# Performance work log

Measured on AMD Instinct MI355X. Metric: run time of the kernel, lower is better.

Reference implementation:

```python
import jax, jax.numpy as jnp
import numpy as np

T, B, S, D = 512, 32, 512, 512
EPS = 1e-6  # LayerNorm eps


def _ln(x, g, b):
    m = jnp.mean(x, axis=-1, keepdims=True)
    v = jnp.mean((x - m) ** 2, axis=-1, keepdims=True)
    return g * (x - m) * jax.lax.rsqrt(v + EPS) + b


def setup_inputs() -> dict:
    key = jax.random.key(0)
    ks = jax.random.split(key, 10)
    sc = 1.0 / np.sqrt(D).astype(np.float32)
    return {
        "prev_layer": jax.random.normal(ks[0], (T, B, D), jnp.float32),
        "hidden": jax.random.normal(ks[1], (B, D), jnp.float32),
        "enc_output": jax.random.normal(ks[2], (B, S, D), jnp.float32),
        "memory_length": jax.random.randint(ks[3], (B,), 1, S + 1),
        # nn.Linear weights stored as [in, out] (transposed torch layout)
        "W_in": jax.random.normal(ks[4], (D, 3 * D), jnp.float32) * sc,
        "W_enc": jax.random.normal(ks[5], (D, D), jnp.float32) * sc,
        "W_attn_in": jax.random.normal(ks[6], (D, D), jnp.float32) * sc,
        "W_hidden": jax.random.normal(ks[7], (D, D), jnp.float32) * sc,
        "W_ctx": jax.random.normal(ks[8], (D, D), jnp.float32) * sc,
        # LayerNorm gains/biases (5 LNs)
        "g_pre": jnp.ones((3 * D,), jnp.float32), "b_pre": jnp.zeros((3 * D,), jnp.float32),
        "g_enc": jnp.ones((D,), jnp.float32), "b_enc": jnp.zeros((D,), jnp.float32),
        "g_attn": jnp.ones((D,), jnp.float32), "b_attn": jnp.zeros((D,), jnp.float32),
        "g_h": jnp.ones((D,), jnp.float32), "b_h": jnp.zeros((D,), jnp.float32),
        "g_c": jnp.ones((D,), jnp.float32), "b_c": jnp.zeros((D,), jnp.float32),
    }


def reference(prev_layer, hidden, enc_output, W_in, W_enc, W_attn_in, W_hidden,
              W_ctx, g_pre, b_pre, g_enc, b_enc, g_attn, b_attn, g_h, b_h,
              g_c, b_c, memory_length):
    d = prev_layer.shape[-1]
    sqrt_d = jnp.sqrt(jnp.asarray(d, prev_layer.dtype))
    # dropout is identity in eval mode
    preact = _ln(prev_layer @ W_in, g_pre, b_pre)          # [T,B,3D]
    pctx = _ln(enc_output @ W_enc, g_enc, b_enc)           # [B,S,D]
    z, h_gate, pl_t = jnp.split(preact, 3, axis=-1)
    z = jax.nn.sigmoid(z)
    h_gate = jax.nn.sigmoid(h_gate)

    # SRU-style linear recurrence: s_t = (1-z_t)*s_{t-1} + z_t*pl_t
    def step(h, zp):
        z_t, p_t = zp
        s = (1.0 - z_t) * h + z_t * p_t
        return s, s

    hidden_last, ss = jax.lax.scan(step, hidden, (z, pl_t))  # ss: [T,B,D]

    attn_in = _ln(ss @ W_attn_in, g_attn, b_attn)            # [T,B,D]
    align = jnp.einsum('tbd,bsd->bts', attn_in, pctx)        # [B,T,S]
    mask = jnp.arange(pctx.shape[1])[None, :] < memory_length[:, None]  # [B,S]
    align = jnp.where(mask[:, None, :], align, -jnp.inf)
    av = jax.nn.softmax(align / sqrt_d, axis=-1)             # [B,T,S]
    c = jnp.einsum('bts,bsd->tbd', av, pctx)                 # [T,B,D]
    attn_out = c / sqrt_d

    trans = _ln(ss @ W_hidden, g_h, b_h) + _ln(attn_out @ W_ctx, g_c, b_c)
    out = jnp.tanh(trans)
    out = (1.0 - h_gate) * out + h_gate * prev_layer         # [T,B,D]
    p_attn = jnp.transpose(av, (1, 0, 2))                    # [T,B,S]
    return out, hidden_last, p_attn
```

## Files before the change

### kernel.cpp

```cpp
#include <hip/hip_runtime.h>
#include <hip/hip_bf16.h>
#include <cmath>

#define T_ 512
#define B_ 32
#define S_ 512
#define D_ 512
#define D3_ 1536
#define NCH 16
#define CT (T_ / NCH)
static constexpr float LN_EPS = 1e-6f;
static constexpr float RSQRT_D = 0.044194173824159216f;

typedef __attribute__((ext_vector_type(8))) __bf16 bf16x8;
typedef __attribute__((ext_vector_type(4))) float f32x4;

struct __align__(8) bfx4 { __hip_bfloat16 x, y, z, w; };
struct __align__(16) u16x8 { unsigned short h[8]; };

__device__ __forceinline__ void g2l16(const void* g, void* l) {
    __builtin_amdgcn_global_load_lds(
        (const __attribute__((address_space(1))) unsigned int*)g,
        (__attribute__((address_space(3))) unsigned int*)l, 16, 0, 0);
}

__device__ __forceinline__ float xr_sum16(float v) {
    v += __shfl_xor(v, 1); v += __shfl_xor(v, 2);
    v += __shfl_xor(v, 4); v += __shfl_xor(v, 8); return v;
}
__device__ __forceinline__ float xr_max16(float v) {
    v = fmaxf(v, __shfl_xor(v, 1)); v = fmaxf(v, __shfl_xor(v, 2));
    v = fmaxf(v, __shfl_xor(v, 4)); v = fmaxf(v, __shfl_xor(v, 8)); return v;
}

__device__ __forceinline__ float sigmoidf_(float x) {
    return 1.f / (1.f + __expf(-x));
}
__device__ __forceinline__ float sigmoid_fast(float x) {
    return __fdividef(1.f, 1.f + __expf(-x));
}
__device__ __forceinline__ float tanh_fast(float x) {
    return 1.f - __fdividef(2.f, __expf(2.f * x) + 1.f);
}
__device__ __forceinline__ float bfu(unsigned short u) {
    unsigned int v = ((unsigned int)u) << 16;
    return __uint_as_float(v);
}

__global__ __launch_bounds__(256) void gemm_pre(
    const __hip_bfloat16* __restrict__ A,
    const __hip_bfloat16* __restrict__ Bw,
    __hip_bfloat16* __restrict__ preb,
    float2* __restrict__ part)
{
    __shared__ char smem[32768];

    const int lin = blockIdx.y * 12 + blockIdx.x;
    const int swz = (lin & 7) * 192 + (lin >> 3);
    const int bx = swz % 12, by = swz / 12;
    const int m0 = by * 128, n0 = bx * 128;
    const int tid = threadIdx.x, lane = tid & 63, w = tid >> 6;
    const int wm = (w >> 1) * 64, wn = (w & 1) * 64;
    const int srow = lane >> 2, skB = (lane & 3) * 16;
    const int q = lane >> 4, c = lane & 15;

    f32x4 acc[4][4];
#pragma unroll
    for (int i = 0; i < 4; i++)
#pragma unroll
        for (int j = 0; j < 4; j++) acc[i][j] = (f32x4)(0.0f);

    const char* ga0 = (const char*)(A + (long)(m0 + w * 16 + srow) * 512) + skB;
    const char* ga1 = (const char*)(A + (long)(m0 + (w + 4) * 16 + srow) * 512) + skB;
    const char* gb0 = (const char*)(Bw + (long)(n0 + w * 16 + srow) * 512) + skB;
    const char* gb1 = (const char*)(Bw + (long)(n0 + (w + 4) * 16 + srow) * 512) + skB;
    char* la0 = smem + w * 1024 + lane * 16;
    char* la1 = smem + (w + 4) * 1024 + lane * 16;
    char* lb0 = smem + 8192 + w * 1024 + lane * 16;
    char* lb1 = smem + 8192 + (w + 4) * 1024 + lane * 16;
    const char* Ar = smem + (wm + c) * 64 + q * 16;
    const char* Br = smem + 8192 + (wn + c) * 64 + q * 16;

    g2l16(ga0, la0);
    g2l16(ga1, la1);
    g2l16(gb0, lb0);
    g2l16(gb1, lb1);
    __syncthreads();

#pragma unroll
    for (int kk = 0; kk < 16; kk++) {
        const int cb = (kk & 1) << 14;
        const int nb = cb ^ 16384;
        if (kk < 15) {
            const long kb = (long)(kk + 1) * 64;
            g2l16(ga0 + kb, la0 + nb);
            g2l16(ga1 + kb, la1 + nb);
            g2l16(gb0 + kb, lb0 + nb);
            g2l16(gb1 + kb, lb1 + nb);
        }
        bf16x8 af[4], bfr[4];
#pragma unroll
        for (int i = 0; i < 4; i++) {
            af[i] = *(const bf16x8*)(Ar + cb + i * 1024);
            bfr[i] = *(const bf16x8*)(Br + cb + i * 1024);
        }
#pragma unroll
        for (int i = 0; i < 4; i++)
#pragma unroll
            for (int j = 0; j < 4; j++)
                acc[i][j] = __builtin_amdgcn_mfma_f32_16x16x32_bf16(
                    af[i], bfr[j], acc[i][j], 0, 0, 0);
        __syncthreads();
    }

    float2* sred = (float2*)smem;
#pragma unroll
    for (int i = 0; i < 4; i++)
#pragma unroll
        for (int r = 0; r < 4; r++) {
            float s = 0.f, qq = 0.f;
#pragma unroll
            for (int j = 0; j < 4; j++) {
                float v = acc[i][j][r]; s += v; qq += v * v;
            }
            s = xr_sum16(s); qq = xr_sum16(qq);
            if (c == 0) sred[(wm + i * 16 + q * 4 + r) * 2 + (w & 1)] =
                make_float2(s, qq);
        }
    __syncthreads();
    if ((w & 1) == 0 && c == 0) {
#pragma unroll
        for (int i = 0; i < 4; i++)
#pragma unroll
            for (int r = 0; r < 4; r++) {
                int row = wm + i * 16 + q * 4 + r;
                float2 a = sred[row * 2], b2 = sred[row * 2 + 1];
                part[(long)bx * 16384 + m0 + row] =
                    make_float2(a.x + b2.x, a.y + b2.y);
            }
    }
    __syncthreads();

    for (int p = 0; p < 2; p++) {
        if ((w >> 1) == p) {
#pragma unroll
            for (int i = 0; i < 4; i++)
#pragma unroll
                for (int j = 0; j < 4; j++)
#pragma unroll
                    for (int r = 0; r < 4; r++) {
                        int row = i * 16 + q * 4 + r;
                        int col = wn + j * 16 + c;
                        ((__hip_bfloat16*)smem)[row * 128 + col] =
                            __float2bfloat16(acc[i][j][r]);
                    }
        }
        __syncthreads();
#pragma unroll
        for (int rnd = 0; rnd < 4; rnd++) {
            int row = rnd * 16 + (tid >> 4);
            int ch = tid & 15;
            uint4 v = *(const uint4*)(smem + row * 256 + ch * 16);
            long grow = m0 + p * 64 + row;
            *(uint4*)((char*)preb + grow * 3072 + (long)n0 * 2 + ch * 16) = v;
        }
        __syncthreads();
    }
}

__global__ __launch_bounds__(256) void g128(
    const __hip_bfloat16* __restrict__ A, long ldaE,
    const __hip_bfloat16* __restrict__ Bw, long bStrideZ,
    __hip_bfloat16* __restrict__ out, long outStrideB,
    float2* __restrict__ part, float scale, int swizzle)
{
    __shared__ char smem[32768];
    int bx, by;
    if (gridDim.z > 1) {
        bx = blockIdx.x; by = blockIdx.y;
        A += (long)blockIdx.z * 512;
        Bw += (long)blockIdx.z * bStrideZ;
        out += (long)blockIdx.z * 512;
    } else if (swizzle) {
        const int nwg = gridDim.x * gridDim.y;
        const int lin = blockIdx.y * gridDim.x + blockIdx.x;
        const int cpx = nwg >> 3;
        const int swz = (lin & 7) * cpx + (lin >> 3);
        bx = swz % gridDim.x; by = swz / gridDim.x;
    } else { bx = blockIdx.x; by = blockIdx.y; }

    const int m0 = by * 128, n0 = bx * 128;
    const int tid = threadIdx.x, lane = tid & 63, w = tid >> 6;
    const int wm = (w >> 1) * 64, wn = (w & 1) * 64;
    const int srow = lane >> 2, skB = (lane & 3) * 16;
    const int q = lane >> 4, c = lane & 15;

    f32x4 acc[4][4];
#pragma unroll
    for (int i = 0; i < 4; i++)
#pragma unroll
        for (int j = 0; j < 4; j++) acc[i][j] = (f32x4)(0.0f);

    const char* ga0 = (const char*)(A + (long)(m0 + w * 16 + srow) * ldaE) + skB;
    const char* ga1 = (const char*)(A + (long)(m0 + (w + 4) * 16 + srow) * ldaE) + skB;
    const char* gb0 = (const char*)(Bw + (long)(n0 + w * 16 + srow) * 512) + skB;
    const char* gb1 = (const char*)(Bw + (long)(n0 + (w + 4) * 16 + srow) * 512) + skB;
    char* la0 = smem + w * 1024 + lane * 16;
    char* la1 = smem + (w + 4) * 1024 + lane * 16;
    char* lb0 = smem + 8192 + w * 1024 + lane * 16;
    char* lb1 = smem + 8192 + (w + 4) * 1024 + lane * 16;
    const char* Ar = smem + (wm + c) * 64 + q * 16;
    const char* Br = smem + 8192 + (wn + c) * 64 + q * 16;

    g2l16(ga0, la0);
    g2l16(ga1, la1);
    g2l16(gb0, lb0);
    g2l16(gb1, lb1);
    __syncthreads();

#pragma unroll
    for (int kk = 0; kk < 16; kk++) {
        const int cb = (kk & 1) << 14;
        const int nb = cb ^ 16384;
        if (kk < 15) {
            const long kb = (long)(kk + 1) * 64;
            g2l16(ga0 + kb, la0 + nb);
            g2l16(ga1 + kb, la1 + nb);
            g2l16(gb0 + kb, lb0 + nb);
            g2l16(gb1 + kb, lb1 + nb);
        }
        bf16x8 af[4], bfr[4];
#pragma unroll
        for (int i = 0; i < 4; i++) {
            af[i] = *(const bf16x8*)(Ar + cb + i * 1024);
            bfr[i] = *(const bf16x8*)(Br + cb + i * 1024);
        }
#pragma unroll
        for (int i = 0; i < 4; i++)
#pragma unroll
            for (int j = 0; j < 4; j++)
                acc[i][j] = __builtin_amdgcn_mfma_f32_16x16x32_bf16(
                    af[i], bfr[j], acc[i][j], 0, 0, 0);
        __syncthreads();
    }

    if (part) {
        float2* sred = (float2*)smem;
#pragma unroll
        for (int i = 0; i < 4; i++)
#pragma unroll
            for (int r = 0; r < 4; r++) {
                float s = 0.f, qq = 0.f;
#pragma unroll
                for (int j = 0; j < 4; j++) {
                    float v = acc[i][j][r]; s += v; qq += v * v;
                }
                s = xr_sum16(s); qq = xr_sum16(qq);
                if (c == 0) sred[(wm + i * 16 + q * 4 + r) * 2 + (w & 1)] =
                    make_float2(s, qq);
            }
        __syncthreads();
        if ((w & 1) == 0 && c == 0) {
#pragma unroll
            for (int i = 0; i < 4; i++)
#pragma unroll
                for (int r = 0; r < 4; r++) {
                    int row = wm + i * 16 + q * 4 + r;
                    float2 a = sred[row * 2], b2 = sred[row * 2 + 1];
                    part[(long)bx * 16384 + m0 + row] =
                        make_float2(a.x + b2.x, a.y + b2.y);
                }
        }
        __syncthreads();
    }

    for (int p = 0; p < 2; p++) {
        if ((w >> 1) == p) {
#pragma unroll
            for (int i = 0; i < 4; i++)
#pragma unroll
                for (int j = 0; j < 4; j++)
#pragma unroll
                    for (int r = 0; r < 4; r++) {
                        int row = i * 16 + q * 4 + r;
                        int col = wn + j * 16 + c;
                        ((__hip_bfloat16*)smem)[row * 128 + col] =
                            __float2bfloat16(acc[i][j][r] * scale);
                    }
        }
        __syncthreads();
#pragma unroll
        for (int rnd = 0; rnd < 4; rnd++) {
            int row = rnd * 16 + (tid >> 4);
            int ch = tid & 15;
            uint4 v = *(const uint4*)(smem + row * 256 + ch * 16);
            long grow = m0 + p * 64 + row;
            *(uint4*)((char*)out + grow * outStrideB + (long)n0 * 2 + ch * 16) = v;
        }
        __syncthreads();
    }
}

#define RC_BUF 34816
__device__ __forceinline__ void rows_core32_lds(
    const __hip_bfloat16* A, long lda,
    const __hip_bfloat16* B, long ldb,
    char* smem, f32x4 (&acc)[2][8])
{
    const int tid = threadIdx.x, lane = tid & 63, w = tid >> 6;
#pragma unroll
    for (int m = 0; m < 2; m++)
#pragma unroll
        for (int j = 0; j < 8; j++) acc[m][j] = (f32x4)(0.0f);

    const char* ga = (const char*)(A + (long)(w * 16 + (lane >> 2)) * lda) + (lane & 3) * 16;
    char* la = smem + w * 1024 + lane * 16;
    const char* gb = (const char*)(B + (long)(w * 128 + (lane >> 2)) * ldb) + (lane & 3) * 16;
    char* lb = smem + 2048 + w * 8192 + lane * 16;
    const long ldbB16 = (long)ldb * 32;
    const char* Ar = smem + (lane & 15) * 64 + (lane >> 4) * 16;
    const char* Br = smem + 2048 + (w * 128 + (lane & 15)) * 64 + (lane >> 4) * 16;

    if (w < 2) g2l16(ga, la);
#pragma unroll
    for (int s = 0; s < 8; s++) g2l16(gb + s * ldbB16, lb + s * 1024);
    __syncthreads();

#pragma unroll
    for (int kk = 0; kk < 16; kk++) {
        const int cb = (kk & 1) * RC_BUF;
        const int nb = ((kk & 1) ^ 1) * RC_BUF;
        if (kk < 15) {
            const long kb = (long)(kk + 1) * 64;
            if (w < 2) g2l16(ga + kb, la + nb);
#pragma unroll
            for (int s = 0; s < 8; s++)
                g2l16(gb + kb + s * ldbB16, lb + nb + s * 1024);
        }
        bf16x8 af[2], bfr[8];
#pragma unroll
        for (int m = 0; m < 2; m++) af[m] = *(const bf16x8*)(Ar + cb + m * 1024);
#pragma unroll
        for (int j = 0; j < 8; j++) bfr[j] = *(const bf16x8*)(Br + cb + j * 1024);
#pragma unroll
        for (int m = 0; m < 2; m++)
#pragma unroll
            for (int j = 0; j < 8; j++)
                acc[m][j] = __builtin_amdgcn_mfma_f32_16x16x32_bf16(
                    af[m], bfr[j], acc[m][j], 0, 0, 0);
        __syncthreads();
    }
}

__global__ __launch_bounds__(256, 2) void gemm_attn(
    const __hip_bfloat16* __restrict__ attninC2,
    const __hip_bfloat16* __restrict__ pctxb,
    const int* __restrict__ mlen,
    float* __restrict__ pattn, __hip_bfloat16* __restrict__ softb)
{
    __shared__ char smem[69632];
    const int b = blockIdx.z;
    const long t0 = (long)blockIdx.y * 32;
    f32x4 acc[2][8];
    rows_core32_lds(attninC2 + (long)b * 1024 + t0 * 32768, 32768,
                    pctxb + (long)b * 262144, 512, smem, acc);

    const int tid = threadIdx.x, lane = tid & 63, w = tid >> 6;
    const int q = lane >> 4, c = lane & 15;
    const int len = mlen[b];
    float* sred = (float*)smem;

#pragma unroll
    for (int m = 0; m < 2; m++)
#pragma unroll
        for (int r = 0; r < 4; r++) {
            float mx = -INFINITY;
#pragma unroll
            for (int j = 0; j < 8; j++) {
                int col = w * 128 + j * 16 + c;
                float v = acc[m][j][r] * RSQRT_D;
                acc[m][j][r] = v;
                if (col < len) mx = fmaxf(mx, v);
            }
            mx = xr_max16(mx);
            if (c == 0) sred[(m * 16 + q * 4 + r) * 4 + w] = mx;
        }
    __syncthreads();
    float rmax[2][4];
#pragma unroll
    for (int m = 0; m < 2; m++)
#pragma unroll
        for (int r = 0; r < 4; r++) {
            int row = m * 16 + q * 4 + r;
            rmax[m][r] = fmaxf(fmaxf(sred[row * 4], sred[row * 4 + 1]),
                               fmaxf(sred[row * 4 + 2], sred[row * 4 + 3]));
        }
    __syncthreads();
#pragma unroll
    for (int m = 0; m < 2; m++)
#pragma unroll
        for (int r = 0; r < 4; r++) {
            float s = 0.f;
#pragma unroll
            for (int j = 0; j < 8; j++) {
                int col = w * 128 + j * 16 + c;
                float e = (col < len) ? __expf(acc[m][j][r] - rmax[m][r]) : 0.f;
                acc[m][j][r] = e; s += e;
            }
            s = xr_sum16(s);
            if (c == 0) sred[(m * 16 + q * 4 + r) * 4 + w] = s;
        }
    __syncthreads();
    float rinv[2][4];
#pragma unroll
    for (int m = 0; m < 2; m++)
#pragma unroll
        for (int r = 0; r < 4; r++) {
            int row = m * 16 + q * 4 + r;
            rinv[m][r] = 1.f / (sred[row * 4] + sred[row * 4 + 1] +
                                sred[row * 4 + 2] + sred[row * 4 + 3]);
        }
    __syncthreads();

#pragma unroll
    for (int m = 0; m < 2; m++)
#pragma unroll
        for (int j = 0; j < 8; j++)
#pragma unroll
            for (int r = 0; r < 4; r++) {
                int row = m * 16 + q * 4 + r;
                int col = w * 128 + j * 16 + c;
                float p = acc[m][j][r] * rinv[m][r];
                acc[m][j][r] = p;
                pattn[((t0 + row) * 32 + b) * 512 + col] = p;
                ((__hip_bfloat16*)smem)[row * 512 + col] = __float2bfloat16(p);
            }
    __syncthreads();
#pragma unroll
    for (int rnd = 0; rnd < 8; rnd++) {
        int row = rnd * 4 + w;
        uint4 v = *(const uint4*)(smem + row * 1024 + lane * 16);
        *(uint4*)((char*)softb + ((t0 + row) * 32 + b) * 1024 + lane * 16) = v;
    }
}

__global__ __launch_bounds__(256) void stats4(
    const float2* __restrict__ part, float2* __restrict__ st)
{
    int r = blockIdx.x * 256 + threadIdx.x;
    float s = 0.f, qq = 0.f;
#pragma unroll
    for (int cb = 0; cb < 4; cb++) {
        float2 v = part[(long)cb * 16384 + r]; s += v.x; qq += v.y;
    }
    float m = s * (1.f / 512);
    float rs = rsqrtf(qq * (1.f / 512) - m * m + LN_EPS);
    st[r] = make_float2(m, rs);
}

__global__ __launch_bounds__(256) void ln_apply_s(
    __hip_bfloat16* __restrict__ x,
    const float2* __restrict__ st,
    const float* __restrict__ g, const float* __restrict__ bb)
{
    int i = blockIdx.x * 256 + threadIdx.x;
    int row = i >> 6;
    int c0 = (i & 63) * 8;
    float2 s = st[row];
    char* p = (char*)x + (long)row * 2048 + (long)(i & 63) * 16;
    u16x8 v = *(const u16x8*)p;
    float4 g0 = *(const float4*)(g + c0), g1 = *(const float4*)(g + c0 + 4);
    float4 b0 = *(const float4*)(bb + c0), b1 = *(const float4*)(bb + c0 + 4);
    float gv[8] = {g0.x, g0.y, g0.z, g0.w, g1.x, g1.y, g1.z, g1.w};
    float bv[8] = {b0.x, b0.y, b0.z, b0.w, b1.x, b1.y, b1.z, b1.w};
#pragma unroll
    for (int k = 0; k < 8; k++) {
        float f = (bfu(v.h[k]) - s.x) * s.y * gv[k] + bv[k];
        v.h[k] = __hip_bfloat16_raw(__float2bfloat16(f)).x;
    }
    *(u16x8*)p = v;
}

__global__ __launch_bounds__(256) void lnt(
    __hip_bfloat16* __restrict__ x,
    __hip_bfloat16* __restrict__ xT,
    const float2* __restrict__ st,
    const float* __restrict__ g, const float* __restrict__ bb)
{
    long boff = (long)blockIdx.z * (S_ * D_);
    int d0 = blockIdx.x * 32, s0 = blockIdx.y * 32;
    __shared__ __hip_bfloat16 t[32][34];
    int tx = threadIdx.x & 31, ty = threadIdx.x >> 5;
    float gv = g[d0 + tx], bv = bb[d0 + tx];
#pragma unroll
    for (int i = 0; i < 4; i++) {
        int srow = s0 + ty + i * 8;
        long row = (long)blockIdx.z * S_ + srow;
        float2 s = st[row];
        float f = (bfu(__hip_bfloat16_raw(x[boff + (long)srow * D_ + d0 + tx]).x)
                   - s.x) * s.y * gv + bv;
        __hip_bfloat16 h = __float2bfloat16(f);
        t[ty + i * 8][tx] = h;
        x[boff + (long)srow * D_ + d0 + tx] = h;
    }
    __syncthreads();
#pragma unroll
    for (int i = 0; i < 4; i++)
        xT[boff + (long)(d0 + ty + i * 8) * S_ + s0 + tx] = t[tx][ty + i * 8];
}

__global__ __launch_bounds__(256) void fin_ep(
    const __hip_bfloat16* __restrict__ h2r,
    const __hip_bfloat16* __restrict__ C2,
    const __hip_bfloat16* __restrict__ preb,
    const float2* __restrict__ st_c, const float2* __restrict__ st_h,
    const float2* __restrict__ st_p,
    const float* __restrict__ g_c, const float* __restrict__ b_c,
    const float* __restrict__ g_h, const float* __restrict__ b_h,
    const float* __restrict__ g_pre, const float* __restrict__ b_pre,
    const float* __restrict__ prev, float* __restrict__ out)
{
    const long m0 = (long)blockIdx.x * 32;
    const int tid = threadIdx.x;
#pragma unroll
    for (int ch = 0; ch < 16; ch++) {
        int f4 = ch * 256 + tid;
        int row = f4 >> 7;
        long rowg = m0 + row;
        int col = (f4 & 127) * 4;
        ushort4 h2 = *(const ushort4*)((const char*)h2r + rowg * 1024 + col * 2);
        ushort4 h1 = *(const ushort4*)((const char*)C2 + rowg * 2048 + 1024 + col * 2);
        ushort4 hr = *(const ushort4*)((const char*)preb + rowg * 3072 + 1024 + col * 2);
        float4 pv = *(const float4*)(prev + rowg * 512 + col);
        float4 gc = *(const float4*)(g_c + col), bc = *(const float4*)(b_c + col);
        float4 gh = *(const float4*)(g_h + col), bh = *(const float4*)(b_h + col);
        float4 gp = *(const float4*)(g_pre + 512 + col);
        float4 bp = *(const float4*)(b_pre + 512 + col);
        float2 sc = st_c[rowg], sh = st_h[rowg], sp = st_p[rowg];
        auto fuse = [&](unsigned short h2u, unsigned short h1u, unsigned short hru,
                        float pvv, float gcv, float bcv, float ghv, float bhv,
                        float gpv, float bpv) -> float {
            float t2 = (bfu(h2u) - sc.x) * sc.y * gcv + bcv;
            float t1 = (bfu(h1u) - sh.x) * sh.y * ghv + bhv;
            float hg = sigmoid_fast((bfu(hru) - sp.x) * sp.y * gpv + bpv);
            return (1.f - hg) * tanh_fast(t1 + t2) + hg * pvv;
        };
        float4 o;
        o.x = fuse(h2.x, h1.x, hr.x, pv.x, gc.x, bc.x, gh.x, bh.x, gp.x, bp.x);
        o.y = fuse(h2.y, h1.y, hr.y, pv.y, gc.y, bc.y, gh.y, bh.y, gp.y, bp.y);
        o.z = fuse(h2.z, h1.z, hr.z, pv.z, gc.z, bc.z, gh.z, bh.z, gp.z, bp.z);
        o.w = fuse(h2.w, h1.w, hr.w, pv.w, gc.w, bc.w, gh.w, bh.w, gp.w, bp.w);
        *(float4*)(out + rowg * 512 + col) = o;
    }
}

__global__ __launch_bounds__(256) void cvt4(
    const float* __restrict__ x, __hip_bfloat16* __restrict__ y, int n4)
{
    int i = blockIdx.x * 256 + threadIdx.x;
    if (i >= n4) return;
    float4 v = ((const float4*)x)[i];
    bfx4 o;
    o.x = __float2bfloat16(v.x); o.y = __float2bfloat16(v.y);
    o.z = __float2bfloat16(v.z); o.w = __float2bfloat16(v.w);
    ((bfx4*)y)[i] = o;
}

__global__ __launch_bounds__(256) void wtrans(
    const float* __restrict__ w0, const float* __restrict__ w1,
    const float* __restrict__ w2, const float* __restrict__ w3,
    const float* __restrict__ w4, __hip_bfloat16* __restrict__ WT)
{
    int z = blockIdx.z;
    const float* W; long off; int N;
    if (z == 0)      { W = w0; off = 0;                N = 1536; }
    else if (z == 1) { W = w1; off = 786432;           N = 512; }
    else if (z == 2) { W = w2; off = 786432 + 262144;  N = 512; }
    else if (z == 3) { W = w3; off = 786432 + 524288;  N = 512; }
    else             { W = w4; off = 786432 + 786432;  N = 512; }
    int n0 = blockIdx.x * 32, k0 = blockIdx.y * 32;
    if (n0 >= N) return;
    __shared__ float t[32][33];
    int tx = threadIdx.x & 31, ty = threadIdx.x >> 5;
#pragma unroll
    for (int i = 0; i < 4; i++)
        t[ty + i * 8][tx] = W[(long)(k0 + ty + i * 8) * N + n0 + tx];
    __syncthreads();
    __hip_bfloat16* O = WT + off;
#pragma unroll
    for (int i = 0; i < 4; i++)
        O[(long)(n0 + ty + i * 8) * 512 + k0 + tx] =
            __float2bfloat16(t[tx][ty + i * 8]);
}

__global__ __launch_bounds__(256) void stats_fin(
    const float2* __restrict__ part, float2* __restrict__ stats)
{
    int r = blockIdx.x * 256 + threadIdx.x;
    float s = 0.f, qq = 0.f;
#pragma unroll
    for (int cb = 0; cb < 12; cb++) {
        float2 v = part[(long)cb * 16384 + r]; s += v.x; qq += v.y;
    }
    float m = s * (1.f / 1536);
    float rs = rsqrtf(qq * (1.f / 1536) - m * m + LN_EPS);
    stats[r] = make_float2(m, rs);
}

__global__ __launch_bounds__(256) void scan_part1(
    const __hip_bfloat16* __restrict__ preb, const float2* __restrict__ stats,
    const float* __restrict__ gpre, const float* __restrict__ bpre,
    float* __restrict__ Ap, float* __restrict__ Bp)
{
    int i2 = blockIdx.x * 256 + threadIdx.x;
    int b = i2 >> 8, d = (i2 & 255) * 2;
    int idx = b * 512 + d;
    int ch = blockIdx.y;
    float2 gz = *(const float2*)(gpre + d), bz = *(const float2*)(bpre + d);
    float2 gp = *(const float2*)(gpre + 1024 + d);
    float2 bp = *(const float2*)(bpre + 1024 + d);
    float A0 = 1.f, s0 = 0.f, A1 = 1.f, s1 = 0.f;
    for (int t = ch * CT; t < (ch + 1) * CT; t++) {
        long row = (long)t * 32 + b;
        float2 st = stats[row];
        ushort2 zr = *(const ushort2*)(preb + row * 1536 + d);
        ushort2 pr = *(const ushort2*)(preb + row * 1536 + 1024 + d);
        float z0 = sigmoidf_((bfu(zr.x) - st.x) * st.y * gz.x + bz.x);
        float z1 = sigmoidf_((bfu(zr.y) - st.x) * st.y * gz.y + bz.y);
        float p0 = (bfu(pr.x) - st.x) * st.y * gp.x + bp.x;
        float p1 = (bfu(pr.y) - st.x) * st.y * gp.y + bp.y;
        A0 *= (1.f - z0); s0 = (1.f - z0) * s0 + z0 * p0;
        A1 *= (1.f - z1); s1 = (1.f - z1) * s1 + z1 * p1;
    }
    *(float2*)(Ap + ch * 16384 + idx) = make_float2(A0, A1);
    *(float2*)(Bp + ch * 16384 + idx) = make_float2(s0, s1);
}

__global__ __launch_bounds__(256) void scan_part2(
    const float* __restrict__ Ap, const float* __restrict__ Bp,
    const float* __restrict__ h0, float* __restrict__ sin_,
    float* __restrict__ hlast)
{
    int idx = blockIdx.x * 256 + threadIdx.x;
    float s = h0[idx];
    for (int ch = 0; ch < NCH; ch++) {
        sin_[ch * 16384 + idx] = s;
        s = Ap[ch * 16384 + idx] * s + Bp[ch * 16384 + idx];
    }
    hlast[idx] = s;
}

__global__ __launch_bounds__(256) void scan_part3(
    const __hip_bfloat16* __restrict__ preb, const float2* __restrict__ stats,
    const float* __restrict__ gpre, const float* __restrict__ bpre,
    const float* __restrict__ sin_, __hip_bfloat16* __restrict__ ssb)
{
    int i2 = blockIdx.x * 256 + threadIdx.x;
    int b = i2 >> 8, d = (i2 & 255) * 2;
    int idx = b * 512 + d;
    int ch = blockIdx.y;
    float2 gz = *(const float2*)(gpre + d), bz = *(const float2*)(bpre + d);
    float2 gp = *(const float2*)(gpre + 1024 + d);
    float2 bp = *(const float2*)(bpre + 1024 + d);
    float2 sv = *(const float2*)(sin_ + ch * 16384 + idx);
    float s0 = sv.x, s1 = sv.y;
    for (int t = ch * CT; t < (ch + 1) * CT; t++) {
        long row = (long)t * 32 + b;
        float2 st = stats[row];
        ushort2 zr = *(const ushort2*)(preb + row * 1536 + d);
        ushort2 pr = *(const ushort2*)(preb + row * 1536 + 1024 + d);
        float z0 = sigmoidf_((bfu(zr.x) - st.x) * st.y * gz.x + bz.x);
        float z1 = sigmoidf_((bfu(zr.y) - st.x) * st.y * gz.y + bz.y);
        float p0 = (bfu(pr.x) - st.x) * st.y * gp.x + bp.x;
        float p1 = (bfu(pr.y) - st.x) * st.y * gp.y + bp.y;
        s0 += z0 * (p0 - s0);
        s1 += z1 * (p1 - s1);
        ushort2 o;
        o.x = __hip_bfloat16_raw(__float2bfloat16(s0)).x;
        o.y = __hip_bfloat16_raw(__float2bfloat16(s1)).x;
        *(ushort2*)(ssb + (long)t * 16384 + idx) = o;
    }
}

extern "C" void kernel_launch(void* const* d_in, const int* in_sizes, int n_in,
                              void* d_out, int out_size, void* d_ws, size_t ws_size,
                              hipStream_t stream) {
    const float* prev  = (const float*)d_in[0];
    const float* hid0  = (const float*)d_in[1];
    const float* enc   = (const float*)d_in[2];
    const int*   mlen  = (const int*)  d_in[3];
    const float* W_in  = (const float*)d_in[4];
    const float* W_enc = (const float*)d_in[5];
    const float* W_att = (const float*)d_in[6];
    const float* W_hid = (const float*)d_in[7];
    const float* W_ctx = (const float*)d_in[8];
    const float* g_pre = (const float*)d_in[9];
    const float* b_pre = (const float*)d_in[10];
    const float* g_enc = (const float*)d_in[11];
    const float* b_enc = (const float*)d_in[12];
    const float* g_att = (const float*)d_in[13];
    const float* b_att = (const float*)d_in[14];
    const float* g_h   = (const float*)d_in[15];
    const float* b_h   = (const float*)d_in[16];
    const float* g_c   = (const float*)d_in[17];
    const float* b_c   = (const float*)d_in[18];

    float* out   = (float*)d_out;
    float* hlast = out + (long)T_ * B_ * D_;
    float* pattn = hlast + (long)B_ * D_;

    char* ws = (char*)d_ws;
    __hip_bfloat16* preb    = (__hip_bfloat16*)(ws);
    __hip_bfloat16* WT      = (__hip_bfloat16*)(ws + 50331648);
    __hip_bfloat16* prevb   = (__hip_bfloat16*)(ws + 54525952);
    __hip_bfloat16* encb    = (__hip_bfloat16*)(ws + 71303168);
    __hip_bfloat16* pctxb   = (__hip_bfloat16*)(ws + 88080384);
    __hip_bfloat16* pctxT   = (__hip_bfloat16*)(ws + 104857600);
    __hip_bfloat16* ssb     = (__hip_bfloat16*)(ws + 121634816);
    __hip_bfloat16* C2      = (__hip_bfloat16*)(ws + 138412032);
    __hip_bfloat16* attnoutb= (__hip_bfloat16*)(ws + 171966464);
    __hip_bfloat16* softb   = (__hip_bfloat16*)(ws + 188743680);
    float2* part            = (float2*)(ws + 205520896);
    float2* stats           = (float2*)(ws + 207093760);
    float* scanA            = (float*)(ws + 207224832);
    float* scanB            = (float*)(ws + 208273408);
    float* sinb             = (float*)(ws + 209321984);
    float2* stats_enc       = (float2*)(ws + 210370560);
    float2* stats_att       = (float2*)(ws + 210501632);
    float2* stats_h         = (float2*)(ws + 210632704);
    float2* stats_c         = (float2*)(ws + 210763776);

    __hip_bfloat16* h2raw = softb;

    const __hip_bfloat16* W_encT = WT + 786432;
    const __hip_bfloat16* W_attT = WT + 786432 + 262144;
    const __hip_bfloat16* W_ctxT = WT + 786432 + 786432;

    dim3 blk(256);

    cvt4<<<8192, blk, 0, stream>>>(prev, prevb, 2097152);
    cvt4<<<8192, blk, 0, stream>>>(enc, encb, 2097152);
    wtrans<<<dim3(48, 16, 5), blk, 0, stream>>>(W_in, W_enc, W_att, W_hid,
                                                W_ctx, WT);

    gemm_pre<<<dim3(12, 128), blk, 0, stream>>>(prevb, WT, preb, part);
    stats_fin<<<64, blk, 0, stream>>>(part, stats);

    scan_part1<<<dim3(32, NCH), blk, 0, stream>>>(preb, stats, g_pre, b_pre,
                                                  scanA, scanB);
    scan_part2<<<64, blk, 0, stream>>>(scanA, scanB, hid0, sinb, hlast);
    scan_part3<<<dim3(32, NCH), blk, 0, stream>>>(preb, stats, g_pre, b_pre,
                                                  sinb, ssb);

    g128<<<dim3(4, 128), blk, 0, stream>>>(encb, 512, W_encT, 0, pctxb, 1024,
                                           part, 1.f, 1);
    stats4<<<64, blk, 0, stream>>>(part, stats_enc);
    lnt<<<dim3(16, 16, 32), blk, 0, stream>>>(pctxb, pctxT, stats_enc,
                                              g_enc, b_enc);

    g128<<<dim3(8, 128), blk, 0, stream>>>(ssb, 512, W_attT, 0, C2, 2048,
                                           part, 1.f, 1);
    stats4<<<64, blk, 0, stream>>>(part, stats_att);
    stats4<<<64, blk, 0, stream>>>(part + 4 * 16384, stats_h);
    ln_apply_s<<<4096, blk, 0, stream>>>(C2, stats_att, g_att, b_att);

    gemm_attn<<<dim3(1, 16, 32), blk, 0, stream>>>(C2, pctxb, mlen,
                                                   pattn, softb);

    g128<<<dim3(4, 4, 32), blk, 0, stream>>>(softb, 16384, pctxT, 262144,
                                             attnoutb, 32768, nullptr,
                                             RSQRT_D, 0);

    g128<<<dim3(4, 128), blk, 0, stream>>>(attnoutb, 512, W_ctxT, 0, h2raw,
                                           1024, part, 1.f, 1);
    stats4<<<64, blk, 0, stream>>>(part, stats_c);

    fin_ep<<<512, blk, 0, stream>>>(h2raw, C2, preb, stats_c, stats_h, stats,
                                    g_c, b_c, g_h, b_h, g_pre, b_pre, prev,
                                    out);
}
```

Measured before the change: 436.2 us.

## Fold W_ctx into LN-encoded context to drop attention-output GEMM

Uses associativity: (av·pctx)·W_ctx = av·(pctx·W_ctx), and pctx·W_ctx is computed as LN-expanded encoder GEMM with a precomputed (g_enc∘W_ctx)-scaled W_enc product plus rank-one correction vectors u,v. The encoder GEMM now produces both pctx and the projected context in one wide GEMM, fused into a single launch with the ss·[W_att|W_hid] GEMM, and the final W_ctx GEMM on attention output is eliminated. It also unifies gemm_pre into the shared g128 body. This trades one T×B×D×D GEMM for a wider encoder GEMM and adds extra bf16 rounding of the fused weights, a numerical risk.

```diff
diff --git a/kernel.cpp b/kernel.cpp
--- a/kernel.cpp
+++ b/kernel.cpp
@@ -6,7 +6,6 @@
 #define B_ 32
 #define S_ 512
 #define D_ 512
-#define D3_ 1536
 #define NCH 16
 #define CT (T_ / NCH)
 static constexpr float LN_EPS = 1e-6f;
@@ -47,148 +46,14 @@
     return __uint_as_float(v);
 }
 
-__global__ __launch_bounds__(256) void gemm_pre(
-    const __hip_bfloat16* __restrict__ A,
+__device__ __forceinline__ void g128_body(
+    const __hip_bfloat16* __restrict__ A, long ldaE,
     const __hip_bfloat16* __restrict__ Bw,
-    __hip_bfloat16* __restrict__ preb,
-    float2* __restrict__ part)
+    __hip_bfloat16* __restrict__ out, long outStrideB,
+    float2* __restrict__ part, int partMul, int partBase,
+    float scale, int bx, int by)
 {
     __shared__ char smem[32768];
-
-    const int lin = blockIdx.y * 12 + blockIdx.x;
-    const int swz = (lin & 7) * 192 + (lin >> 3);
-    const int bx = swz % 12, by = swz / 12;
-    const int m0 = by * 128, n0 = bx * 128;
-    const int tid = threadIdx.x, lane = tid & 63, w = tid >> 6;
-    const int wm = (w >> 1) * 64, wn = (w & 1) * 64;
-    const int srow = lane >> 2, skB = (lane & 3) * 16;
-    const int q = lane >> 4, c = lane & 15;
-
-    f32x4 acc[4][4];
-#pragma unroll
-    for (int i = 0; i < 4; i++)
-#pragma unroll
-        for (int j = 0; j < 4; j++) acc[i][j] = (f32x4)(0.0f);
-
-    const char* ga0 = (const char*)(A + (long)(m0 + w * 16 + srow) * 512) + skB;
-    const char* ga1 = (const char*)(A + (long)(m0 + (w + 4) * 16 + srow) * 512) + skB;
-    const char* gb0 = (const char*)(Bw + (long)(n0 + w * 16 + srow) * 512) + skB;
-    const char* gb1 = (const char*)(Bw + (long)(n0 + (w + 4) * 16 + srow) * 512) + skB;
-    char* la0 = smem + w * 1024 + lane * 16;
-    char* la1 = smem + (w + 4) * 1024 + lane * 16;
-    char* lb0 = smem + 8192 + w * 1024 + lane * 16;
-    char* lb1 = smem + 8192 + (w + 4) * 1024 + lane * 16;
-    const char* Ar = smem + (wm + c) * 64 + q * 16;
-    const char* Br = smem + 8192 + (wn + c) * 64 + q * 16;
-
-    g2l16(ga0, la0);
-    g2l16(ga1, la1);
-    g2l16(gb0, lb0);
-    g2l16(gb1, lb1);
-    __syncthreads();
-
-#pragma unroll
-    for (int kk = 0; kk < 16; kk++) {
-        const int cb = (kk & 1) << 14;
-        const int nb = cb ^ 16384;
-        if (kk < 15) {
-            const long kb = (long)(kk + 1) * 64;
-            g2l16(ga0 + kb, la0 + nb);
-            g2l16(ga1 + kb, la1 + nb);
-            g2l16(gb0 + kb, lb0 + nb);
-            g2l16(gb1 + kb, lb1 + nb);
-        }
-        bf16x8 af[4], bfr[4];
-#pragma unroll
-        for (int i = 0; i < 4; i++) {
-            af[i] = *(const bf16x8*)(Ar + cb + i * 1024);
-            bfr[i] = *(const bf16x8*)(Br + cb + i * 1024);
-        }
-#pragma unroll
-        for (int i = 0; i < 4; i++)
-#pragma unroll
-            for (int j = 0; j < 4; j++)
-                acc[i][j] = __builtin_amdgcn_mfma_f32_16x16x32_bf16(
-                    af[i], bfr[j], acc[i][j], 0, 0, 0);
-        __syncthreads();
-    }
-
-    float2* sred = (float2*)smem;
-#pragma unroll
-    for (int i = 0; i < 4; i++)
-#pragma unroll
-        for (int r = 0; r < 4; r++) {
-            float s = 0.f, qq = 0.f;
-#pragma unroll
-            for (int j = 0; j < 4; j++) {
-                float v = acc[i][j][r]; s += v; qq += v * v;
-            }
-            s = xr_sum16(s); qq = xr_sum16(qq);
-            if (c == 0) sred[(wm + i * 16 + q * 4 + r) * 2 + (w & 1)] =
-                make_float2(s, qq);
-        }
-    __syncthreads();
-    if ((w & 1) == 0 && c == 0) {
-#pragma unroll
-        for (int i = 0; i < 4; i++)
-#pragma unroll
-            for (int r = 0; r < 4; r++) {
-                int row = wm + i * 16 + q * 4 + r;
-                float2 a = sred[row * 2], b2 = sred[row * 2 + 1];
-                part[(long)bx * 16384 + m0 + row] =
-                    make_float2(a.x + b2.x, a.y + b2.y);
-            }
-    }
-    __syncthreads();
-
-    for (int p = 0; p < 2; p++) {
-        if ((w >> 1) == p) {
-#pragma unroll
-            for (int i = 0; i < 4; i++)
-#pragma unroll
-                for (int j = 0; j < 4; j++)
-#pragma unroll
-                    for (int r = 0; r < 4; r++) {
-                        int row = i * 16 + q * 4 + r;
-                        int col = wn + j * 16 + c;
-                        ((__hip_bfloat16*)smem)[row * 128 + col] =
-                            __float2bfloat16(acc[i][j][r]);
-                    }
-        }
-        __syncthreads();
-#pragma unroll
-        for (int rnd = 0; rnd < 4; rnd++) {
-            int row = rnd * 16 + (tid >> 4);
-            int ch = tid & 15;
-            uint4 v = *(const uint4*)(smem + row * 256 + ch * 16);
-            long grow = m0 + p * 64 + row;
-            *(uint4*)((char*)preb + grow * 3072 + (long)n0 * 2 + ch * 16) = v;
-        }
-        __syncthreads();
-    }
-}
-
-__global__ __launch_bounds__(256) void g128(
-    const __hip_bfloat16* __restrict__ A, long ldaE,
-    const __hip_bfloat16* __restrict__ Bw, long bStrideZ,
-    __hip_bfloat16* __restrict__ out, long outStrideB,
-    float2* __restrict__ part, float scale, int swizzle)
-{
-    __shared__ char smem[32768];
-    int bx, by;
-    if (gridDim.z > 1) {
-        bx = blockIdx.x; by = blockIdx.y;
-        A += (long)blockIdx.z * 512;
-        Bw += (long)blockIdx.z * bStrideZ;
-        out += (long)blockIdx.z * 512;
-    } else if (swizzle) {
-        const int nwg = gridDim.x * gridDim.y;
-        const int lin = blockIdx.y * gridDim.x + blockIdx.x;
-        const int cpx = nwg >> 3;
-        const int swz = (lin & 7) * cpx + (lin >> 3);
-        bx = swz % gridDim.x; by = swz / gridDim.x;
-    } else { bx = blockIdx.x; by = blockIdx.y; }
-
     const int m0 = by * 128, n0 = bx * 128;
     const int tid = threadIdx.x, lane = tid & 63, w = tid >> 6;
     const int wm = (w >> 1) * 64, wn = (w & 1) * 64;
@@ -253,7 +118,7 @@
                 float s = 0.f, qq = 0.f;
 #pragma unroll
                 for (int j = 0; j < 4; j++) {
-                    float v = acc[i][j][r]; s += v; qq += v * v;
+                    float v = acc[i][j][r] * scale; s += v; qq += v * v;
                 }
                 s = xr_sum16(s); qq = xr_sum16(qq);
                 if (c == 0) sred[(wm + i * 16 + q * 4 + r) * 2 + (w & 1)] =
@@ -267,7 +132,7 @@
                 for (int r = 0; r < 4; r++) {
                     int row = wm + i * 16 + q * 4 + r;
                     float2 a = sred[row * 2], b2 = sred[row * 2 + 1];
-                    part[(long)bx * 16384 + m0 + row] =
+                    part[(long)bx * 16384 + (long)(m0 + row) * partMul + partBase] =
                         make_float2(a.x + b2.x, a.y + b2.y);
                 }
         }
@@ -299,6 +164,49 @@
         }
         __syncthreads();
     }
+}
+
+__global__ __launch_bounds__(256) void g128(
+    const __hip_bfloat16* __restrict__ A, long ldaE,
+    const __hip_bfloat16* __restrict__ Bw, long bStrideZ,
+    __hip_bfloat16* __restrict__ out, long outStrideB,
+    float2* __restrict__ part, float scale, int swizzle)
+{
+    int bx, by, pmul = 1, pbase = 0;
+    if (gridDim.z > 1) {
+        bx = blockIdx.x; by = blockIdx.y;
+        A += (long)blockIdx.z * 512;
+        Bw += (long)blockIdx.z * bStrideZ;
+        out += (long)blockIdx.z * 512;
+        pmul = 32; pbase = blockIdx.z;
+    } else if (swizzle) {
+        const int nwg = gridDim.x * gridDim.y;
+        const int lin = blockIdx.y * gridDim.x + blockIdx.x;
+        const int cpx = nwg >> 3;
+        const int swz = (lin & 7) * cpx + (lin >> 3);
+        bx = swz % gridDim.x; by = swz / gridDim.x;
+    } else { bx = blockIdx.x; by = blockIdx.y; }
+    g128_body(A, ldaE, Bw, out, outStrideB, part, pmul, pbase, scale, bx, by);
+}
+
+__global__ __launch_bounds__(256) void g128mid(
+    const __hip_bfloat16* __restrict__ encb,
+    const __hip_bfloat16* __restrict__ ssb,
+    const __hip_bfloat16* __restrict__ WE2,
+    const __hip_bfloat16* __restrict__ WAH,
+    __hip_bfloat16* __restrict__ E2, __hip_bfloat16* __restrict__ C2,
+    float2* __restrict__ partA, float2* __restrict__ partB)
+{
+    const int lin = blockIdx.x;
+    const int swz = (lin & 7) * 256 + (lin >> 3);
+    const __hip_bfloat16 *A, *Bw;
+    __hip_bfloat16* out;
+    float2* part;
+    int local;
+    if (swz < 1024) { A = encb; Bw = WE2; out = E2; part = partA; local = swz; }
+    else { A = ssb; Bw = WAH; out = C2; part = partB; local = swz - 1024; }
+    const int bx = local & 7, by = local >> 3;
+    g128_body(A, 512, Bw, out, 2048, part, 1, 0, 1.f, bx, by);
 }
 
 #define RC_BUF 34816
@@ -481,32 +389,34 @@
     *(u16x8*)p = v;
 }
 
-__global__ __launch_bounds__(256) void lnt(
-    __hip_bfloat16* __restrict__ x,
-    __hip_bfloat16* __restrict__ xT,
+__global__ __launch_bounds__(256) void midfix(
+    const __hip_bfloat16* __restrict__ E2,
+    __hip_bfloat16* __restrict__ pctxb, __hip_bfloat16* __restrict__ pwT,
     const float2* __restrict__ st,
-    const float* __restrict__ g, const float* __restrict__ bb)
-{
-    long boff = (long)blockIdx.z * (S_ * D_);
-    int d0 = blockIdx.x * 32, s0 = blockIdx.y * 32;
+    const float* __restrict__ g, const float* __restrict__ bb,
+    const float* __restrict__ uv)
+{
+    const int b = blockIdx.z, d0 = blockIdx.x * 32, s0 = blockIdx.y * 32;
     __shared__ __hip_bfloat16 t[32][34];
-    int tx = threadIdx.x & 31, ty = threadIdx.x >> 5;
-    float gv = g[d0 + tx], bv = bb[d0 + tx];
+    const int tx = threadIdx.x & 31, ty = threadIdx.x >> 5;
+    const float gv = g[d0 + tx], bv = bb[d0 + tx];
+    const float ud = uv[d0 + tx], vd = uv[512 + d0 + tx];
 #pragma unroll
     for (int i = 0; i < 4; i++) {
         int srow = s0 + ty + i * 8;
-        long row = (long)blockIdx.z * S_ + srow;
+        long row = (long)b * 512 + srow;
         float2 s = st[row];
-        float f = (bfu(__hip_bfloat16_raw(x[boff + (long)srow * D_ + d0 + tx]).x)
-                   - s.x) * s.y * gv + bv;
-        __hip_bfloat16 h = __float2bfloat16(f);
-        t[ty + i * 8][tx] = h;
-        x[boff + (long)srow * D_ + d0 + tx] = h;
+        float pc = __bfloat162float(E2[row * 1024 + d0 + tx]);
+        pctxb[row * 512 + d0 + tx] =
+            __float2bfloat16((pc - s.x) * s.y * gv + bv);
+        float pr = __bfloat162float(E2[row * 1024 + 512 + d0 + tx]);
+        t[ty + i * 8][tx] = __float2bfloat16(s.y * pr - s.y * s.x * ud + vd);
     }
     __syncthreads();
 #pragma unroll
     for (int i = 0; i < 4; i++)
-        xT[boff + (long)(d0 + ty + i * 8) * S_ + s0 + tx] = t[tx][ty + i * 8];
+        pwT[(long)b * 262144 + (long)(d0 + ty + i * 8) * 512 + s0 + tx] =
+            t[tx][ty + i * 8];
 }
 
 __global__ __launch_bounds__(256) void fin_ep(
@@ -569,15 +479,16 @@
 __global__ __launch_bounds__(256) void wtrans(
     const float* __restrict__ w0, const float* __restrict__ w1,
     const float* __restrict__ w2, const float* __restrict__ w3,
-    const float* __restrict__ w4, __hip_bfloat16* __restrict__ WT)
+    const float* __restrict__ w4, __hip_bfloat16* __restrict__ WT,
+    __hip_bfloat16* __restrict__ WE2)
 {
     int z = blockIdx.z;
-    const float* W; long off; int N;
-    if (z == 0)      { W = w0; off = 0;                N = 1536; }
-    else if (z == 1) { W = w1; off = 786432;           N = 512; }
-    else if (z == 2) { W = w2; off = 786432 + 262144;  N = 512; }
-    else if (z == 3) { W = w3; off = 786432 + 524288;  N = 512; }
-    else             { W = w4; off = 786432 + 786432;  N = 512; }
+    const float* W; __hip_bfloat16* O; int N;
+    if (z == 0)      { W = w0; O = WT;                          N = 1536; }
+    else if (z == 1) { W = w1; O = WE2;                         N = 512; }
+    else if (z == 2) { W = w2; O = WT + 786432 + 262144;        N = 512; }
+    else if (z == 3) { W = w3; O = WT + 786432 + 524288;        N = 512; }
+    else             { W = w4; O = WT + 786432 + 786432;        N = 512; }
     int n0 = blockIdx.x * 32, k0 = blockIdx.y * 32;
     if (n0 >= N) return;
     __shared__ float t[32][33];
@@ -586,11 +497,32 @@
     for (int i = 0; i < 4; i++)
         t[ty + i * 8][tx] = W[(long)(k0 + ty + i * 8) * N + n0 + tx];
     __syncthreads();
-    __hip_bfloat16* O = WT + off;
 #pragma unroll
     for (int i = 0; i < 4; i++)
         O[(long)(n0 + ty + i * 8) * 512 + k0 + tx] =
             __float2bfloat16(t[tx][ty + i * 8]);
+}
+
+__global__ __launch_bounds__(256) void wgscale(
+    const __hip_bfloat16* __restrict__ wctxT, const float* __restrict__ g,
+    __hip_bfloat16* __restrict__ wgT)
+{
+    int i = blockIdx.x * 256 + threadIdx.x;
+    int d1 = i & 511;
+    wgT[i] = __float2bfloat16(__bfloat162float(wctxT[i]) * g[d1]);
+}
+
+__global__ __launch_bounds__(256) void uvk(
+    const float* __restrict__ Wctx, const float* __restrict__ g,
+    const float* __restrict__ b, float* __restrict__ uv)
+{
+    int d = blockIdx.x * 256 + threadIdx.x;
+    float u = 0.f, v = 0.f;
+    for (int k = 0; k < 512; k++) {
+        float w = Wctx[(long)k * 512 + d];
+        u += g[k] * w; v += b[k] * w;
+    }
+    uv[d] = u; uv[512 + d] = v;
 }
 
 __global__ __launch_bounds__(256) void stats_fin(
@@ -715,24 +647,29 @@
     __hip_bfloat16* prevb   = (__hip_bfloat16*)(ws + 54525952);
     __hip_bfloat16* encb    = (__hip_bfloat16*)(ws + 71303168);
     __hip_bfloat16* pctxb   = (__hip_bfloat16*)(ws + 88080384);
-    __hip_bfloat16* pctxT   = (__hip_bfloat16*)(ws + 104857600);
+    __hip_bfloat16* pwT     = (__hip_bfloat16*)(ws + 104857600);
     __hip_bfloat16* ssb     = (__hip_bfloat16*)(ws + 121634816);
     __hip_bfloat16* C2      = (__hip_bfloat16*)(ws + 138412032);
-    __hip_bfloat16* attnoutb= (__hip_bfloat16*)(ws + 171966464);
-    __hip_bfloat16* softb   = (__hip_bfloat16*)(ws + 188743680);
+    __hip_bfloat16* E2      = (__hip_bfloat16*)(ws + 171966464);
+    __hip_bfloat16* softb   = (__hip_bfloat16*)(ws + 171966464);
+    __hip_bfloat16* h2raw   = (__hip_bfloat16*)(ws + 188743680);
     float2* part            = (float2*)(ws + 205520896);
-    float2* stats           = (float2*)(ws + 207093760);
-    float* scanA            = (float*)(ws + 207224832);
-    float* scanB            = (float*)(ws + 208273408);
-    float* sinb             = (float*)(ws + 209321984);
-    float2* stats_enc       = (float2*)(ws + 210370560);
-    float2* stats_att       = (float2*)(ws + 210501632);
-    float2* stats_h         = (float2*)(ws + 210632704);
-    float2* stats_c         = (float2*)(ws + 210763776);
-
-    __hip_bfloat16* h2raw = softb;
-
-    const __hip_bfloat16* W_encT = WT + 786432;
+    float2* stats           = (float2*)(ws + 207618048);
+    float* scanA            = (float*)(ws + 207749120);
+    float* scanB            = (float*)(ws + 208797696);
+    float* sinb             = (float*)(ws + 209846272);
+    float2* stats_enc       = (float2*)(ws + 210894848);
+    float2* stats_att       = (float2*)(ws + 211025920);
+    float2* stats_h         = (float2*)(ws + 211156992);
+    float2* stats_c         = (float2*)(ws + 211288064);
+    __hip_bfloat16* WE2     = (__hip_bfloat16*)(ws + 211419136);
+    float* uv               = (float*)(ws + 212467712);
+    __hip_bfloat16* WgT     = (__hip_bfloat16*)scanA;
+    __hip_bfloat16* Wencbf  = (__hip_bfloat16*)scanB;
+
+    float2* partA = part;
+    float2* partB = part + 8 * 16384;
+
     const __hip_bfloat16* W_attT = WT + 786432 + 262144;
     const __hip_bfloat16* W_ctxT = WT + 786432 + 786432;
 
@@ -740,10 +677,16 @@
 
     cvt4<<<8192, blk, 0, stream>>>(prev, prevb, 2097152);
     cvt4<<<8192, blk, 0, stream>>>(enc, encb, 2097152);
+    cvt4<<<256, blk, 0, stream>>>(W_enc, Wencbf, 65536);
     wtrans<<<dim3(48, 16, 5), blk, 0, stream>>>(W_in, W_enc, W_att, W_hid,
-                                                W_ctx, WT);
-
-    gemm_pre<<<dim3(12, 128), blk, 0, stream>>>(prevb, WT, preb, part);
+                                                W_ctx, WT, WE2);
+    wgscale<<<1024, blk, 0, stream>>>(W_ctxT, g_enc, WgT);
+    uvk<<<2, blk, 0, stream>>>(W_ctx, g_enc, b_enc, uv);
+    g128<<<dim3(4, 4), blk, 0, stream>>>(WgT, 512, Wencbf, 0, WE2 + 262144,
+                                         1024, nullptr, 1.f, 0);
+
+    g128<<<dim3(12, 128), blk, 0, stream>>>(prevb, 512, WT, 0, preb, 3072,
+                                            part, 1.f, 1);
     stats_fin<<<64, blk, 0, stream>>>(part, stats);
 
     scan_part1<<<dim3(32, NCH), blk, 0, stream>>>(preb, stats, g_pre, b_pre,
@@ -752,27 +695,21 @@
     scan_part3<<<dim3(32, NCH), blk, 0, stream>>>(preb, stats, g_pre, b_pre,
                                                   sinb, ssb);
 
-    g128<<<dim3(4, 128), blk, 0, stream>>>(encb, 512, W_encT, 0, pctxb, 1024,
-                                           part, 1.f, 1);
-    stats4<<<64, blk, 0, stream>>>(part, stats_enc);
-    lnt<<<dim3(16, 16, 32), blk, 0, stream>>>(pctxb, pctxT, stats_enc,
-                                              g_enc, b_enc);
-
-    g128<<<dim3(8, 128), blk, 0, stream>>>(ssb, 512, W_attT, 0, C2, 2048,
-                                           part, 1.f, 1);
-    stats4<<<64, blk, 0, stream>>>(part, stats_att);
-    stats4<<<64, blk, 0, stream>>>(part + 4 * 16384, stats_h);
+    g128mid<<<2048, blk, 0, stream>>>(encb, ssb, WE2, W_attT, E2, C2,
+                                      partA, partB);
+    stats4<<<64, blk, 0, stream>>>(partA, stats_enc);
+    stats4<<<64, blk, 0, stream>>>(partB, stats_att);
+    stats4<<<64, blk, 0, stream>>>(partB + 4 * 16384, stats_h);
+
+    midfix<<<dim3(16, 16, 32), blk, 0, stream>>>(E2, pctxb, pwT, stats_enc,
+                                                 g_enc, b_enc, uv);
     ln_apply_s<<<4096, blk, 0, stream>>>(C2, stats_att, g_att, b_att);
 
     gemm_attn<<<dim3(1, 16, 32), blk, 0, stream>>>(C2, pctxb, mlen,
                                                    pattn, softb);
 
-    g128<<<dim3(4, 4, 32), blk, 0, stream>>>(softb, 16384, pctxT, 262144,
-                                             attnoutb, 32768, nullptr,
-                                             RSQRT_D, 0);
-
-    g128<<<dim3(4, 128), blk, 0, stream>>>(attnoutb, 512, W_ctxT, 0, h2raw,
-                                           1024, part, 1.f, 1);
+    g128<<<dim3(4, 4, 32), blk, 0, stream>>>(softb, 16384, pwT, 262144,
+                                             h2raw, 32768, part, RSQRT_D, 0);
     stats4<<<64, blk, 0, stream>>>(part, stats_c);
 
     fin_ep<<<512, blk, 0, stream>>>(h2raw, C2, preb, stats_c, stats_h, stats,
```

After: 462.3 us. 1.06x slower.
